# Performance work log

Measured on AMD Instinct MI355X. Metric: run time of the kernel, lower is better.

## Reference

```python
import jax, jax.numpy as jnp
import numpy as np

B = 4096          # batch of samples
M = 128           # n_orbitals
F = 32            # n_fermions
H = 512           # hidden_units


def setup_inputs() -> dict:
    key = jax.random.key(0)
    kn, kphi, kw1, kb1, kw2, kb2 = jax.random.split(key, 6)
    # occupancy strings: exactly F ones among M orbitals per sample
    keys = jax.random.split(kn, B)
    occ_idx = jax.vmap(lambda k: jax.random.permutation(k, M)[:F])(keys)  # [B,F]
    n = jnp.zeros((B, M), jnp.float32).at[jnp.arange(B)[:, None], occ_idx].set(1.0)
    # parameters
    Phi = jax.random.normal(kphi, (F, M), jnp.float32) * 0.1
    W1 = jax.random.normal(kw1, (M, H), jnp.float32) / np.sqrt(M)
    b1 = jnp.zeros((H,), jnp.float32)
    W2 = jax.random.normal(kw2, (H, F * M), jnp.float32) / np.sqrt(H)
    b2 = jnp.zeros((F * M,), jnp.float32)
    return {"n": n, "Phi": Phi, "W1": W1, "b1": b1, "W2": W2, "b2": b2}


def reference(n, Phi, W1, b1, W2, b2):
    # backflow MLP: Dense -> tanh -> Dense, reshaped to (F, M) per sample
    h = jnp.tanh(n @ W1 + b1)                       # [B,H]
    bf = (h @ W2 + b2).reshape(-1, F, M)            # [B,F,M]
    kernel = Phi[None] + bf                         # [B,F,M]
    # occupied orbital columns; exactly F ones per row, top_k is stable so
    # indices come out in ascending order (same as jnp.where(n, size=F))
    idx = jax.lax.top_k(n, F)[1]                    # [B,F] int32
    phi = jnp.take_along_axis(kernel, idx[:, None, :], axis=2)  # [B,F,F]
    sign, logabs = jnp.linalg.slogdet(phi)
    return jnp.log(sign.astype(jnp.complex64)) + logabs.astype(jnp.complex64)  # [B] complex
```

## Files before the change

kernel.cpp:

```cpp
#include <hip/hip_runtime.h>
#include <hip/hip_bf16.h>
#include <math.h>

#define B_N 4096
#define M_N 128
#define F_N 32
#define H_N 512
#define NFM 4096

#define WAVE_SYNC() do { \
  asm volatile("s_waitcnt lgkmcnt(0)" ::: "memory"); \
  __builtin_amdgcn_sched_barrier(0); \
} while (0)

__global__ __launch_bounds__(256) void k1_idx_h(
    const float* __restrict__ n, const float* __restrict__ W1,
    const float* __restrict__ b1, float* __restrict__ h_ws,
    unsigned int* __restrict__ mask)
{
  __shared__ int s_idx[F_N];
  __shared__ int s_cnt0;
  const int b = blockIdx.x;
  const int t = threadIdx.x;

  bool p = false;
  int before = 0;
  if (t < 128) {
    float v = n[(size_t)b * M_N + t];
    p = v > 0.5f;
    unsigned long long m = __ballot(p);
    int lane = t & 63;
    before = __popcll(m & ((1ull << lane) - 1ull));
    if (lane == 0) {
      if (t < 64) { mask[b*4+0] = (unsigned)m; mask[b*4+1] = (unsigned)(m>>32); }
      else        { mask[b*4+2] = (unsigned)m; mask[b*4+3] = (unsigned)(m>>32); }
    }
    if (t < 64) {
      if (lane == 0) s_cnt0 = __popcll(m);
      if (p) s_idx[before] = t;
    }
  }
  __syncthreads();
  if (t >= 64 && t < 128 && p) s_idx[s_cnt0 + before] = t;
  __syncthreads();

  #pragma unroll
  for (int cc = 0; cc < 2; ++cc) {
    int c = t + cc * 256;
    float acc = 0.0f;
    #pragma unroll
    for (int j = 0; j < F_N; ++j)
      acc += W1[(size_t)s_idx[j] * H_N + c];
    acc += b1[c];
    h_ws[(size_t)b * H_N + c] = tanhf(acc);
  }
}

__global__ __launch_bounds__(256) void k_w2t(
    const float* __restrict__ W2, float* __restrict__ W2t)
{
  __shared__ float lds[32 * 132];
  const int k = blockIdx.x;
  const int t = threadIdx.x;

  #pragma unroll
  for (int i = 0; i < 4; ++i) {
    int m0 = i * 1024 + t * 4;
    float4 v = *(const float4*)&W2[(size_t)k * NFM + m0];
    int ig = m0 >> 7, c = m0 & 127;
    lds[ig * 132 + c + 0] = v.x;
    lds[ig * 132 + c + 1] = v.y;
    lds[ig * 132 + c + 2] = v.z;
    lds[ig * 132 + c + 3] = v.w;
  }
  __syncthreads();

  const int c  = t >> 1;
  const int ih = (t & 1) * 16;
  float* outp = W2t + (size_t)c * (H_N * F_N) + k * F_N + ih;
  #pragma unroll
  for (int i = 0; i < 4; ++i) {
    int ig = ih + i * 4;
    float4 v = make_float4(lds[(ig + 0) * 132 + c], lds[(ig + 1) * 132 + c],
                           lds[(ig + 2) * 132 + c], lds[(ig + 3) * 132 + c]);
    *(float4*)(outp + i * 4) = v;
  }
}

__global__ __launch_bounds__(256) void k_fill(
    const unsigned int* __restrict__ mask,
    int* __restrict__ bcnt, int* __restrict__ boff,
    int* __restrict__ bent, int* __restrict__ loc)
{
  const int c = blockIdx.x;
  const int t = threadIdx.x;
  const int w = t >> 6, lane = t & 63;
  const int word = c >> 5, bit = c & 31;
  __shared__ int s_wcnt[4];
  __shared__ int s_red[8];
  __shared__ int s_run;

  int cnt_loc = 0, off_loc = 0;
  for (int b = t; b < B_N; b += 256) {
    unsigned m0 = mask[(size_t)b*4+0], m1 = mask[(size_t)b*4+1];
    unsigned m2 = mask[(size_t)b*4+2], m3 = mask[(size_t)b*4+3];
    unsigned wv = (word == 0) ? m0 : (word == 1) ? m1 : (word == 2) ? m2 : m3;
    cnt_loc += (int)((wv >> bit) & 1u);
    int r = __popc(wv & ((1u << bit) - 1u));
    if (word > 0) r += __popc(m0);
    if (word > 1) r += __popc(m1);
    if (word > 2) r += __popc(m2);
    off_loc += r;
  }
  #pragma unroll
  for (int off = 32; off > 0; off >>= 1) {
    cnt_loc += __shfl_down(cnt_loc, off);
    off_loc += __shfl_down(off_loc, off);
  }
  if (lane == 0) { s_red[w] = cnt_loc; s_red[4 + w] = off_loc; }
  __syncthreads();
  const int cnt_tot = s_red[0] + s_red[1] + s_red[2] + s_red[3];
  const int off_tot = s_red[4] + s_red[5] + s_red[6] + s_red[7];
  if (t == 0) { bcnt[c] = cnt_tot; boff[c] = off_tot; s_run = 0; }
  __syncthreads();

  for (int chunk = 0; chunk < B_N; chunk += 256) {
    const int b = chunk + t;
    unsigned m0 = mask[(size_t)b*4+0], m1 = mask[(size_t)b*4+1];
    unsigned m2 = mask[(size_t)b*4+2], m3 = mask[(size_t)b*4+3];
    unsigned wv = (word == 0) ? m0 : (word == 1) ? m1 : (word == 2) ? m2 : m3;
    bool p = (wv >> bit) & 1u;
    int j = __popc(wv & ((1u << bit) - 1u));
    if (word > 0) j += __popc(m0);
    if (word > 1) j += __popc(m1);
    if (word > 2) j += __popc(m2);

    unsigned long long bal = __ballot(p);
    int before = __popcll(bal & ((1ull << lane) - 1ull));
    if (lane == 0) s_wcnt[w] = __popcll(bal);
    __syncthreads();
    int wbase = s_run;
    for (int i = 0; i < w; ++i) wbase += s_wcnt[i];
    if (p) {
      int pos = wbase + before;
      bent[(size_t)c * B_N + pos] = (b << 5) | j;
      loc[b * 32 + j] = off_tot + pos;
    }
    __syncthreads();
    if (t == 0) s_run += s_wcnt[0] + s_wcnt[1] + s_wcnt[2] + s_wcnt[3];
    __syncthreads();
  }
}

__global__ __launch_bounds__(256) void k2_gemm_gather(
    const float* __restrict__ h, const float* __restrict__ W2t,
    const float* __restrict__ b2, const float* __restrict__ Phi,
    const int* __restrict__ bcnt, const int* __restrict__ boff,
    const int* __restrict__ bent, float* __restrict__ phi_bucket)
{
  __shared__ __align__(16) float smem[2 * 2624];
  __shared__ int s_b[128];

  const int tid = threadIdx.x;
  const int c   = blockIdx.x;
  const int cnt = bcnt[c];
  const int t0  = blockIdx.y * 128;
  if (t0 >= cnt) return;
  const int base = boff[c];
  const float* w2tc = W2t + (size_t)c * (H_N * F_N);

  if (tid < 128) {
    int ii = t0 + tid;
    int e  = bent[(size_t)c * B_N + (ii < cnt ? ii : cnt - 1)];
    s_b[tid] = e >> 5;
  }
  __syncthreads();

  const int kA  = tid & 15;
  const int rbA = (tid >> 4) * 8;
  const int tx  = tid & 7;
  const int tyr = tid >> 3;

  int rowb[8];
  #pragma unroll
  for (int i = 0; i < 8; ++i) rowb[i] = s_b[rbA + i];

  float acc[4][4];
  #pragma unroll
  for (int i = 0; i < 4; ++i)
    #pragma unroll
    for (int u = 0; u < 4; ++u) acc[i][u] = 0.f;

  float aReg[8], bReg0, bReg1;

  #pragma unroll
  for (int i = 0; i < 8; ++i)
    aReg[i] = h[(size_t)rowb[i] * H_N + kA];
  bReg0 = w2tc[tid];
  bReg1 = w2tc[256 + tid];
  *(float4*)&smem[kA * 132 + rbA] =
      make_float4(aReg[0], aReg[1], aReg[2], aReg[3]);
  *(float4*)&smem[kA * 132 + rbA + 4] =
      make_float4(aReg[4], aReg[5], aReg[6], aReg[7]);
  smem[2112 + tid] = bReg0;
  smem[2112 + 256 + tid] = bReg1;
  __syncthreads();

  #pragma unroll 1
  for (int t = 0; t < 32; ++t) {
    float* Atc = smem + (t & 1) * 2624;
    float* Btc = Atc + 2112;
    float* Atn = smem + ((t + 1) & 1) * 2624;
    float* Btn = Atn + 2112;

    if (t < 31) {
      int k0n = (t + 1) * 16;
      #pragma unroll
      for (int i = 0; i < 8; ++i)
        aReg[i] = h[(size_t)rowb[i] * H_N + k0n + kA];
      bReg0 = w2tc[k0n * 32 + tid];
      bReg1 = w2tc[k0n * 32 + 256 + tid];
    }

    #pragma unroll
    for (int kk = 0; kk < 16; ++kk) {
      float4 av = *(const float4*)&Atc[kk * 132 + tyr * 4];
      float4 bv = *(const float4*)&Btc[kk * 32 + tx * 4];
      float a4[4] = {av.x, av.y, av.z, av.w};
      float b4[4] = {bv.x, bv.y, bv.z, bv.w};
      #pragma unroll
      for (int i = 0; i < 4; ++i)
        #pragma unroll
        for (int u = 0; u < 4; ++u)
          acc[i][u] = fmaf(a4[i], b4[u], acc[i][u]);
    }

    if (t < 31) {
      *(float4*)&Atn[kA * 132 + rbA] =
          make_float4(aReg[0], aReg[1], aReg[2], aReg[3]);
      *(float4*)&Atn[kA * 132 + rbA + 4] =
          make_float4(aReg[4], aReg[5], aReg[6], aReg[7]);
      Btn[tid] = bReg0;
      Btn[256 + tid] = bReg1;
      __syncthreads();
    }
  }

  #pragma unroll
  for (int i = 0; i < 4; ++i) {
    int r = tyr * 4 + i;
    if (t0 + r < cnt) {
      int col = base + t0 + r;
      float v[4];
      #pragma unroll
      for (int u = 0; u < 4; ++u) {
        int ig   = tx * 4 + u;
        int colw = ig * M_N + c;
        v[u] = Phi[colw] + (acc[i][u] + b2[colw]);
      }
      *(float4*)&phi_bucket[(size_t)col * 32 + tx * 4] =
          make_float4(v[0], v[1], v[2], v[3]);
    }
  }
}

__global__ __launch_bounds__(256) void k3_det(
    const float* __restrict__ phi_bucket, const int* __restrict__ loc,
    float* __restrict__ out)
{
  __shared__ float A[4][32 * 33];
  const int w = threadIdx.x >> 6;
  const int lane = threadIdx.x & 63;
  const int b = blockIdx.x * 4 + w;
  float* Aw = A[w];

  {
    const int jj = lane & 31;
    const int hi = lane >> 5;
    int lcol = loc[b * 32 + jj];
    const float* colp = phi_bucket + (size_t)lcol * 32 + hi * 16;
    #pragma unroll
    for (int i = 0; i < 4; ++i) {
      float4 v = *(const float4*)(colp + i * 4);
      int ig = hi * 16 + i * 4;
      Aw[(ig + 0) * 33 + jj] = v.x;
      Aw[(ig + 1) * 33 + jj] = v.y;
      Aw[(ig + 2) * 33 + jj] = v.z;
      Aw[(ig + 3) * 33 + jj] = v.w;
    }
  }
  WAVE_SYNC();

  float logabs = 0.f;
  int negs = 0;
  for (int k = 0; k < 32; ++k) {
    float v = -1.f;
    int vi = lane;
    if (lane >= k && lane < 32) v = fabsf(Aw[lane * 33 + k]);
    #pragma unroll
    for (int off = 32; off > 0; off >>= 1) {
      float ov = __shfl_xor(v, off);
      int oi = __shfl_xor(vi, off);
      if (ov > v || (ov == v && oi < vi)) { v = ov; vi = oi; }
    }
    int p = vi;
    if (p != k) {
      negs ^= 1;
      if (lane < 32) {
        float tmp = Aw[k * 33 + lane];
        Aw[k * 33 + lane] = Aw[p * 33 + lane];
        Aw[p * 33 + lane] = tmp;
      }
    }
    WAVE_SYNC();
    float piv = Aw[k * 33 + k];
    if (piv < 0.f) negs ^= 1;
    logabs += logf(fabsf(piv));
    if (lane > k && lane < 32) {
      float l = Aw[lane * 33 + k];
      if (fabsf(piv) >= 1.17549435e-38f) l = l * (1.0f / piv);
      else                               l = l / piv;
      Aw[lane * 33 + k] = l;
    }
    WAVE_SYNC();
    {
      const int mid = (k + 33) >> 1;
      const int j   = lane & 31;
      const int ilo = (lane < 32) ? (k + 1) : mid;
      const int ihi = (lane < 32) ? mid : 32;
      if (j > k) {
        float nukj = -Aw[k * 33 + j];
        for (int i = ilo; i < ihi; ++i)
          Aw[i * 33 + j] = fmaf(nukj, Aw[i * 33 + k], Aw[i * 33 + j]);
      }
    }
    WAVE_SYNC();
  }

  if (lane == 0) {
    out[b]       = logabs;
    out[B_N + b] = (negs & 1) ? 3.14159265358979f : 0.0f;
  }
}

extern "C" void kernel_launch(void* const* d_in, const int* in_sizes, int n_in,
                              void* d_out, int out_size, void* d_ws, size_t ws_size,
                              hipStream_t stream) {
  const float* n   = (const float*)d_in[0];
  const float* Phi = (const float*)d_in[1];
  const float* W1  = (const float*)d_in[2];
  const float* b1  = (const float*)d_in[3];
  const float* W2  = (const float*)d_in[4];
  const float* b2  = (const float*)d_in[5];
  float* out = (float*)d_out;

  char* ws = (char*)d_ws;
  float*        h_ws       = (float*)ws;
  float*        phi_bucket = (float*)(ws + (size_t)8  * 1024 * 1024);
  float*        W2t        = (float*)(ws + (size_t)24 * 1024 * 1024);
  unsigned int* mask       = (unsigned int*)(ws + (size_t)32 * 1024 * 1024);
  int*          bent       = (int*)(ws + (size_t)32 * 1024 * 1024 + 65536);
  int*          loc        = (int*)(ws + (size_t)34 * 1024 * 1024 + 65536);
  int*          bcnt       = (int*)(ws + (size_t)34 * 1024 * 1024 + 65536 + 524288);
  int*          boff       = (int*)(ws + (size_t)34 * 1024 * 1024 + 65536 + 524288 + 4096);

  hipLaunchKernelGGL(k_w2t, dim3(H_N), dim3(256), 0, stream, W2, W2t);
  hipLaunchKernelGGL(k1_idx_h, dim3(B_N), dim3(256), 0, stream,
                     n, W1, b1, h_ws, mask);
  hipLaunchKernelGGL(k_fill, dim3(M_N), dim3(256), 0, stream,
                     mask, bcnt, boff, bent, loc);
  hipLaunchKernelGGL(k2_gemm_gather, dim3(M_N, 32), dim3(256), 0, stream,
                     h_ws, W2t, b2, Phi, bcnt, boff, bent, phi_bucket);
  hipLaunchKernelGGL(k3_det, dim3(B_N / 4), dim3(256), 0, stream,
                     phi_bucket, loc, out);
}
```

Baseline: 183.2 us.

## Merge W2 transpose with hidden-layer kernel and precompute bucket-fill prefix offsets

Fuses the W2 transpose and the first-layer/tanh kernel into one launch. Blocks 0-511 transpose W2 and the remaining blocks each handle two samples, with float4 loads of W1 rows. In k_fill, per-wave ballot counts from the first pass are stored and turned into a prefix table once. This removes the three __syncthreads per chunk in the scatter loop. It also makes a cosmetic change to an LDS store address in the GEMM kernel. The aim is fewer launches, fewer barriers and wider memory accesses, at the cost of a larger LDS footprint in the merged kernel.

```diff
diff --git a/kernel.cpp b/kernel.cpp
--- a/kernel.cpp
+++ b/kernel.cpp
@@ -13,78 +13,81 @@
   __builtin_amdgcn_sched_barrier(0); \
 } while (0)
 
-__global__ __launch_bounds__(256) void k1_idx_h(
+__global__ __launch_bounds__(256) void k_pre(
     const float* __restrict__ n, const float* __restrict__ W1,
-    const float* __restrict__ b1, float* __restrict__ h_ws,
+    const float* __restrict__ b1, const float* __restrict__ W2,
+    float* __restrict__ W2t, float* __restrict__ h_ws,
     unsigned int* __restrict__ mask)
 {
-  __shared__ int s_idx[F_N];
-  __shared__ int s_cnt0;
-  const int b = blockIdx.x;
+  __shared__ float s_buf[32 * 132];
+  __shared__ int s_idx[2][F_N];
+  __shared__ int s_cnt0[2];
+
   const int t = threadIdx.x;
 
-  bool p = false;
-  int before = 0;
-  if (t < 128) {
-    float v = n[(size_t)b * M_N + t];
-    p = v > 0.5f;
+  if (blockIdx.x < 512) {
+    const int k = blockIdx.x;
+    #pragma unroll
+    for (int i = 0; i < 4; ++i) {
+      int m0 = i * 1024 + t * 4;
+      float4 v = *(const float4*)&W2[(size_t)k * NFM + m0];
+      int ig = m0 >> 7, c = m0 & 127;
+      s_buf[ig * 132 + c + 0] = v.x;
+      s_buf[ig * 132 + c + 1] = v.y;
+      s_buf[ig * 132 + c + 2] = v.z;
+      s_buf[ig * 132 + c + 3] = v.w;
+    }
+    __syncthreads();
+    const int c  = t >> 1;
+    const int ih = (t & 1) * 16;
+    float* outp = W2t + (size_t)c * (H_N * F_N) + k * F_N + ih;
+    #pragma unroll
+    for (int i = 0; i < 4; ++i) {
+      int ig = ih + i * 4;
+      float4 v = make_float4(s_buf[(ig+0)*132 + c], s_buf[(ig+1)*132 + c],
+                             s_buf[(ig+2)*132 + c], s_buf[(ig+3)*132 + c]);
+      *(float4*)(outp + i * 4) = v;
+    }
+    return;
+  }
+
+  const int half = t >> 7;
+  const int tl   = t & 127;
+  const int b    = (blockIdx.x - 512) * 2 + half;
+  const int lane = t & 63;
+
+  {
+    float v = n[(size_t)b * M_N + tl];
+    bool p = v > 0.5f;
     unsigned long long m = __ballot(p);
-    int lane = t & 63;
-    before = __popcll(m & ((1ull << lane) - 1ull));
+    int before = __popcll(m & ((1ull << lane) - 1ull));
     if (lane == 0) {
-      if (t < 64) { mask[b*4+0] = (unsigned)m; mask[b*4+1] = (unsigned)(m>>32); }
-      else        { mask[b*4+2] = (unsigned)m; mask[b*4+3] = (unsigned)(m>>32); }
-    }
-    if (t < 64) {
-      if (lane == 0) s_cnt0 = __popcll(m);
-      if (p) s_idx[before] = t;
-    }
-  }
-  __syncthreads();
-  if (t >= 64 && t < 128 && p) s_idx[s_cnt0 + before] = t;
-  __syncthreads();
-
-  #pragma unroll
-  for (int cc = 0; cc < 2; ++cc) {
-    int c = t + cc * 256;
-    float acc = 0.0f;
-    #pragma unroll
-    for (int j = 0; j < F_N; ++j)
-      acc += W1[(size_t)s_idx[j] * H_N + c];
-    acc += b1[c];
-    h_ws[(size_t)b * H_N + c] = tanhf(acc);
-  }
-}
-
-__global__ __launch_bounds__(256) void k_w2t(
-    const float* __restrict__ W2, float* __restrict__ W2t)
-{
-  __shared__ float lds[32 * 132];
-  const int k = blockIdx.x;
-  const int t = threadIdx.x;
-
-  #pragma unroll
-  for (int i = 0; i < 4; ++i) {
-    int m0 = i * 1024 + t * 4;
-    float4 v = *(const float4*)&W2[(size_t)k * NFM + m0];
-    int ig = m0 >> 7, c = m0 & 127;
-    lds[ig * 132 + c + 0] = v.x;
-    lds[ig * 132 + c + 1] = v.y;
-    lds[ig * 132 + c + 2] = v.z;
-    lds[ig * 132 + c + 3] = v.w;
-  }
-  __syncthreads();
-
-  const int c  = t >> 1;
-  const int ih = (t & 1) * 16;
-  float* outp = W2t + (size_t)c * (H_N * F_N) + k * F_N + ih;
-  #pragma unroll
-  for (int i = 0; i < 4; ++i) {
-    int ig = ih + i * 4;
-    float4 v = make_float4(lds[(ig + 0) * 132 + c], lds[(ig + 1) * 132 + c],
-                           lds[(ig + 2) * 132 + c], lds[(ig + 3) * 132 + c]);
-    *(float4*)(outp + i * 4) = v;
-  }
+      int w2 = (tl < 64) ? 0 : 2;
+      mask[b*4 + w2 + 0] = (unsigned)m;
+      mask[b*4 + w2 + 1] = (unsigned)(m >> 32);
+    }
+    if (tl < 64) {
+      if (lane == 0) s_cnt0[half] = __popcll(m);
+      if (p) s_idx[half][before] = tl;
+    }
+    __syncthreads();
+    if (tl >= 64 && p) s_idx[half][s_cnt0[half] + before] = tl;
+    __syncthreads();
+  }
+
+  const int c0 = tl * 4;
+  float4 acc = make_float4(0.f, 0.f, 0.f, 0.f);
+  #pragma unroll
+  for (int j = 0; j < F_N; ++j) {
+    float4 wv = *(const float4*)&W1[(size_t)s_idx[half][j] * H_N + c0];
+    acc.x += wv.x; acc.y += wv.y; acc.z += wv.z; acc.w += wv.w;
+  }
+  float4 bv = *(const float4*)&b1[c0];
+  acc.x = tanhf(acc.x + bv.x);
+  acc.y = tanhf(acc.y + bv.y);
+  acc.z = tanhf(acc.z + bv.z);
+  acc.w = tanhf(acc.w + bv.w);
+  *(float4*)&h_ws[(size_t)b * H_N + c0] = acc;
 }
 
 __global__ __launch_bounds__(256) void k_fill(
@@ -96,20 +99,25 @@
   const int t = threadIdx.x;
   const int w = t >> 6, lane = t & 63;
   const int word = c >> 5, bit = c & 31;
-  __shared__ int s_wcnt[4];
+  __shared__ int s_wcnt[64];
+  __shared__ int s_pre[64];
   __shared__ int s_red[8];
-  __shared__ int s_run;
 
   int cnt_loc = 0, off_loc = 0;
-  for (int b = t; b < B_N; b += 256) {
+  #pragma unroll 1
+  for (int ch = 0; ch < 16; ++ch) {
+    const int b = ch * 256 + t;
     unsigned m0 = mask[(size_t)b*4+0], m1 = mask[(size_t)b*4+1];
     unsigned m2 = mask[(size_t)b*4+2], m3 = mask[(size_t)b*4+3];
     unsigned wv = (word == 0) ? m0 : (word == 1) ? m1 : (word == 2) ? m2 : m3;
-    cnt_loc += (int)((wv >> bit) & 1u);
+    bool p = (wv >> bit) & 1u;
     int r = __popc(wv & ((1u << bit) - 1u));
     if (word > 0) r += __popc(m0);
     if (word > 1) r += __popc(m1);
     if (word > 2) r += __popc(m2);
+    unsigned long long bal = __ballot(p);
+    if (lane == 0) s_wcnt[ch * 4 + w] = __popcll(bal);
+    cnt_loc += (int)p;
     off_loc += r;
   }
   #pragma unroll
@@ -121,11 +129,17 @@
   __syncthreads();
   const int cnt_tot = s_red[0] + s_red[1] + s_red[2] + s_red[3];
   const int off_tot = s_red[4] + s_red[5] + s_red[6] + s_red[7];
-  if (t == 0) { bcnt[c] = cnt_tot; boff[c] = off_tot; s_run = 0; }
+  if (t == 0) {
+    bcnt[c] = cnt_tot; boff[c] = off_tot;
+    int run = 0;
+    #pragma unroll
+    for (int i = 0; i < 64; ++i) { s_pre[i] = run; run += s_wcnt[i]; }
+  }
   __syncthreads();
 
-  for (int chunk = 0; chunk < B_N; chunk += 256) {
-    const int b = chunk + t;
+  #pragma unroll 1
+  for (int ch = 0; ch < 16; ++ch) {
+    const int b = ch * 256 + t;
     unsigned m0 = mask[(size_t)b*4+0], m1 = mask[(size_t)b*4+1];
     unsigned m2 = mask[(size_t)b*4+2], m3 = mask[(size_t)b*4+3];
     unsigned wv = (word == 0) ? m0 : (word == 1) ? m1 : (word == 2) ? m2 : m3;
@@ -134,21 +148,13 @@
     if (word > 0) j += __popc(m0);
     if (word > 1) j += __popc(m1);
     if (word > 2) j += __popc(m2);
-
     unsigned long long bal = __ballot(p);
     int before = __popcll(bal & ((1ull << lane) - 1ull));
-    if (lane == 0) s_wcnt[w] = __popcll(bal);
-    __syncthreads();
-    int wbase = s_run;
-    for (int i = 0; i < w; ++i) wbase += s_wcnt[i];
     if (p) {
-      int pos = wbase + before;
+      int pos = s_pre[ch * 4 + w] + before;
       bent[(size_t)c * B_N + pos] = (b << 5) | j;
       loc[b * 32 + j] = off_tot + pos;
     }
-    __syncthreads();
-    if (t == 0) s_run += s_wcnt[0] + s_wcnt[1] + s_wcnt[2] + s_wcnt[3];
-    __syncthreads();
   }
 }
 
@@ -236,7 +242,7 @@
     }
 
     if (t < 31) {
-      *(float4*)&Atn[kA * 132 + rbA] =
+      *(float4*)&smem[((t + 1) & 1) * 2624 + kA * 132 + rbA] =
           make_float4(aReg[0], aReg[1], aReg[2], aReg[3]);
       *(float4*)&Atn[kA * 132 + rbA + 4] =
           make_float4(aReg[4], aReg[5], aReg[6], aReg[7]);
@@ -364,9 +370,8 @@
   int*          bcnt       = (int*)(ws + (size_t)34 * 1024 * 1024 + 65536 + 524288);
   int*          boff       = (int*)(ws + (size_t)34 * 1024 * 1024 + 65536 + 524288 + 4096);
 
-  hipLaunchKernelGGL(k_w2t, dim3(H_N), dim3(256), 0, stream, W2, W2t);
-  hipLaunchKernelGGL(k1_idx_h, dim3(B_N), dim3(256), 0, stream,
-                     n, W1, b1, h_ws, mask);
+  hipLaunchKernelGGL(k_pre, dim3(512 + B_N / 2), dim3(256), 0, stream,
+                     n, W1, b1, W2, W2t, h_ws, mask);
   hipLaunchKernelGGL(k_fill, dim3(M_N), dim3(256), 0, stream,
                      mask, bcnt, boff, bent, loc);
   hipLaunchKernelGGL(k2_gemm_gather, dim3(M_N, 32), dim3(256), 0, stream,
```

Result: faster. 179.5 us (-2.1%).
